# Kernel optimization log

Hardware: AMD Instinct MI355X
Metric: run time of the kernel (lower is better)

Reference implementation:

```python
import jax, jax.numpy as jnp
import numpy as np

N_NODES = 50000
N_EDGES = 800000
D_FEAT = 128
D_EMB = 128


def _spmm(row, col, val, x, n):
    # y[i] = sum_{e: row[e]==i} val[e] * x[col[e]]  -- COO spmm via gather + segment_sum
    return jax.ops.segment_sum(val[:, None] * x[col], row, num_segments=n)


def setup_inputs() -> dict:
    key = jax.random.key(0)
    k1, k2, k3, k4, k5 = jax.random.split(key, 5)
    feature = jax.random.normal(k1, (N_NODES, D_FEAT), dtype=jnp.float32)
    adj_row = jax.random.randint(k2, (N_EDGES,), 0, N_NODES, dtype=jnp.int32)
    adj_col = jax.random.randint(k3, (N_EDGES,), 0, N_NODES, dtype=jnp.int32)
    adj_val = jax.random.uniform(k4, (N_EDGES,), dtype=jnp.float32)
    stdv = 1.0 / np.sqrt(D_EMB)
    weight = jax.random.uniform(k5, (D_FEAT, D_EMB), minval=-stdv, maxval=stdv, dtype=jnp.float32)
    return {"feature": feature, "adj_row": adj_row, "adj_col": adj_col,
            "adj_val": adj_val, "weight": weight}


def reference(feature, adj_row, adj_col, adj_val, weight):
    n = feature.shape[0]
    h = _spmm(adj_row, adj_col, adj_val, feature, n)   # adj @ feature
    h = _spmm(adj_row, adj_col, adj_val, h, n)         # adj @ (adj @ feature)
    out = 0.5 * h - 0.5 * feature                      # elementwise combine
    return out @ weight                                # dense projection [N, D_EMB]
```

## Files before the change

### kernel.cpp

```cpp
#include <hip/hip_runtime.h>
#include <hip/hip_fp16.h>

#define D 128
#define SCAT_EPT 16
#define CAP 48

typedef _Float16 f16;
typedef f16 f16x8 __attribute__((ext_vector_type(8)));
typedef float f32x4 __attribute__((ext_vector_type(4)));


__global__ __launch_bounds__(256) void conv_init_kernel(
    const float* __restrict__ x, __half* __restrict__ xh,
    const float* __restrict__ W, __half* __restrict__ Wt,
    int* __restrict__ cnt, long n8, int N) {
  long i = (long)blockIdx.x * blockDim.x + threadIdx.x;
  if (i < n8) {
    const float4* src = reinterpret_cast<const float4*>(x) + i * 2;
    float4 a = src[0], b = src[1];
    __half2 h0 = __floats2half2_rn(a.x, a.y);
    __half2 h1 = __floats2half2_rn(a.z, a.w);
    __half2 h2 = __floats2half2_rn(b.x, b.y);
    __half2 h3 = __floats2half2_rn(b.z, b.w);
    uint4 st;
    st.x = *reinterpret_cast<uint*>(&h0);
    st.y = *reinterpret_cast<uint*>(&h1);
    st.z = *reinterpret_cast<uint*>(&h2);
    st.w = *reinterpret_cast<uint*>(&h3);
    *(reinterpret_cast<uint4*>(xh) + i) = st;
  }
  if (i < D * D) {
    int k = (int)(i >> 7), j = (int)(i & 127);
    Wt[((long)j << 7) + k] = __float2half_rn(W[i]);
  }
  if (i < N) cnt[i] = 0;
}


__global__ __launch_bounds__(256) void build_part_kernel(
    const int* __restrict__ row, const int* __restrict__ col,
    const float* __restrict__ val, int* __restrict__ cnt,
    int2* __restrict__ csrB, int E, int N) {
  const int g = blockIdx.x & 7;
  const int chunk = blockIdx.x >> 3;
  const int gsize = (N + 7) >> 3;
  const int rlo = g * gsize;
  const int rhi = rlo + gsize;
  int i = chunk * (256 * SCAT_EPT) + threadIdx.x;
#pragma unroll
  for (int t = 0; t < SCAT_EPT; ++t, i += 256) {
    if (i < E) {
      int r = row[i];
      if (r >= rlo && r < rhi) {
        int p = atomicAdd(&cnt[r], 1);
        if (p < CAP) csrB[(long)r * CAP + p] = make_int2(col[i], __float_as_int(val[i]));
      }
    }
  }
}


__device__ __forceinline__ float2 row_accum_wave(const int2* __restrict__ cv,
                                                 long s, long e,
                                                 const __half* __restrict__ xh,
                                                 int lane) {
  float2 acc = {0.f, 0.f};
  const int loff = lane << 1;
  long k = s;
  const long e8 = s + ((e - s) & ~7L);
  for (; k < e8; k += 8) {
    int2 c0 = cv[k + 0], c1 = cv[k + 1], c2 = cv[k + 2], c3 = cv[k + 3];
    int2 c4 = cv[k + 4], c5 = cv[k + 5], c6 = cv[k + 6], c7 = cv[k + 7];
    uint u0 = *reinterpret_cast<const uint*>(xh + ((long)c0.x << 7) + loff);
    uint u1 = *reinterpret_cast<const uint*>(xh + ((long)c1.x << 7) + loff);
    uint u2 = *reinterpret_cast<const uint*>(xh + ((long)c2.x << 7) + loff);
    uint u3 = *reinterpret_cast<const uint*>(xh + ((long)c3.x << 7) + loff);
    uint u4 = *reinterpret_cast<const uint*>(xh + ((long)c4.x << 7) + loff);
    uint u5 = *reinterpret_cast<const uint*>(xh + ((long)c5.x << 7) + loff);
    uint u6 = *reinterpret_cast<const uint*>(xh + ((long)c6.x << 7) + loff);
    uint u7 = *reinterpret_cast<const uint*>(xh + ((long)c7.x << 7) + loff);
#define ACC1(uu, cc)                                            \
    {                                                           \
      __half2 h = *reinterpret_cast<__half2*>(&(uu));           \
      float2 f = __half22float2(h);                             \
      float v = __int_as_float((cc).y);                         \
      acc.x = fmaf(v, f.x, acc.x);                              \
      acc.y = fmaf(v, f.y, acc.y);                              \
    }
    ACC1(u0, c0) ACC1(u1, c1) ACC1(u2, c2) ACC1(u3, c3)
    ACC1(u4, c4) ACC1(u5, c5) ACC1(u6, c6) ACC1(u7, c7)
  }
  for (; k < e; ++k) {
    int2 c = cv[k];
    uint u = *reinterpret_cast<const uint*>(xh + ((long)c.x << 7) + loff);
    ACC1(u, c)
  }
#undef ACC1
  return acc;
}


__global__ __launch_bounds__(256) void spmm1_kernel(
    const int* __restrict__ cnt, const int2* __restrict__ csrB,
    const __half* __restrict__ xh, __half* __restrict__ y, int N) {
  int r = blockIdx.x * 4 + (threadIdx.x >> 6);
  int lane = threadIdx.x & 63;
  if (r >= N) return;
  int deg = __builtin_amdgcn_readfirstlane(min(cnt[r], CAP));
  long s = (long)r * CAP;
  float2 acc = row_accum_wave(csrB, s, s + deg, xh, lane);
  __half2 p = __floats2half2_rn(acc.x, acc.y);
  *reinterpret_cast<__half2*>(y + ((long)r << 7) + (lane << 1)) = p;
}


__global__ __launch_bounds__(256) void spmm2z_kernel(
    const int* __restrict__ cnt, const int2* __restrict__ csrB,
    const __half* __restrict__ h1, const float* __restrict__ feat,
    __half* __restrict__ zh, int N) {
  int r = blockIdx.x * 4 + (threadIdx.x >> 6);
  int lane = threadIdx.x & 63;
  if (r >= N) return;
  int deg = __builtin_amdgcn_readfirstlane(min(cnt[r], CAP));
  long s = (long)r * CAP;
  float2 acc = row_accum_wave(csrB, s, s + deg, h1, lane);
  float2 fv = *reinterpret_cast<const float2*>(feat + ((long)r << 7) + (lane << 1));
  __half2 p = __floats2half2_rn(0.5f * (acc.x - fv.x), 0.5f * (acc.y - fv.y));
  *reinterpret_cast<__half2*>(zh + ((long)r << 7) + (lane << 1)) = p;
}


__global__ __launch_bounds__(256) void gemmz_mfma_kernel(
    const __half* __restrict__ zh, const __half* __restrict__ Wt,
    float* __restrict__ out, int N) {
  const int w = threadIdx.x >> 6;
  const int l = threadIdx.x & 63;
  const int r0 = blockIdx.x * 64 + w * 16;
  const int lr = l & 15;
  const int lk = (l >> 4) * 8;

  f16x8 a[4];
  const f16* zp = reinterpret_cast<const f16*>(zh) + ((long)(r0 + lr) << 7) + lk;
#pragma unroll
  for (int ks = 0; ks < 4; ++ks)
    a[ks] = *reinterpret_cast<const f16x8*>(zp + ks * 32);

  const int orow = r0 + (l >> 4) * 4;
#pragma unroll
  for (int jt = 0; jt < 8; ++jt) {
    const f16* wp = reinterpret_cast<const f16*>(Wt) + ((long)(jt * 16 + lr) << 7) + lk;
    f16x8 b0 = *reinterpret_cast<const f16x8*>(wp + 0);
    f16x8 b1 = *reinterpret_cast<const f16x8*>(wp + 32);
    f16x8 b2 = *reinterpret_cast<const f16x8*>(wp + 64);
    f16x8 b3 = *reinterpret_cast<const f16x8*>(wp + 96);
    f32x4 acc = {0.f, 0.f, 0.f, 0.f};
    acc = __builtin_amdgcn_mfma_f32_16x16x32_f16(a[0], b0, acc, 0, 0, 0);
    acc = __builtin_amdgcn_mfma_f32_16x16x32_f16(a[1], b1, acc, 0, 0, 0);
    acc = __builtin_amdgcn_mfma_f32_16x16x32_f16(a[2], b2, acc, 0, 0, 0);
    acc = __builtin_amdgcn_mfma_f32_16x16x32_f16(a[3], b3, acc, 0, 0, 0);
#pragma unroll
    for (int i = 0; i < 4; ++i) {
      int r = orow + i;
      if (r < N) out[((long)r << 7) + jt * 16 + lr] = acc[i];
    }
  }
}


__global__ __launch_bounds__(256) void spmm_atomic_kernel(
    const int* __restrict__ row, const int* __restrict__ col,
    const float* __restrict__ val, const float* __restrict__ x,
    float* __restrict__ y, int E) {
  long idx = (long)blockIdx.x * blockDim.x + threadIdx.x;
  int e = (int)(idx >> 5);
  if (e >= E) return;
  int q = (int)(idx & 31);
  int r = row[e];
  int c = col[e];
  float v = val[e];
  const float4 xv = *reinterpret_cast<const float4*>(x + (long)c * D + q * 4);
  float* yp = y + (long)r * D + q * 4;
  atomicAdd(yp + 0, v * xv.x);
  atomicAdd(yp + 1, v * xv.y);
  atomicAdd(yp + 2, v * xv.z);
  atomicAdd(yp + 3, v * xv.w);
}

__global__ __launch_bounds__(256) void combine_gemm_kernel(
    const float* __restrict__ h2, const float* __restrict__ feat,
    const float* __restrict__ W, float* __restrict__ out, int N) {
  __shared__ float Xs[32][D];
  const int t = threadIdx.x;
  const int rb = blockIdx.x * 32;
#pragma unroll
  for (int i = 0; i < 4; ++i) {
    int o = i * 1024 + t * 4;
    int r = o >> 7;
    int cc = o & 127;
    float4 xv = {0.f, 0.f, 0.f, 0.f};
    if (rb + r < N) {
      float4 hv = *reinterpret_cast<const float4*>(h2 + (long)(rb + r) * D + cc);
      float4 fv = *reinterpret_cast<const float4*>(feat + (long)(rb + r) * D + cc);
      xv.x = 0.5f * (hv.x - fv.x);
      xv.y = 0.5f * (hv.y - fv.y);
      xv.z = 0.5f * (hv.z - fv.z);
      xv.w = 0.5f * (hv.w - fv.w);
    }
    *reinterpret_cast<float4*>(&Xs[r][cc]) = xv;
  }
  __syncthreads();
  const int j0 = (t & 31) * 4;
  const int i0 = (t >> 5) * 4;
  float4 acc[4];
#pragma unroll
  for (int ii = 0; ii < 4; ++ii) acc[ii] = {0.f, 0.f, 0.f, 0.f};
#pragma unroll 8
  for (int kb = 0; kb < 32; ++kb) {
    float4 xr[4], wr[4];
#pragma unroll
    for (int ii = 0; ii < 4; ++ii)
      xr[ii] = *reinterpret_cast<const float4*>(&Xs[i0 + ii][kb * 4]);
#pragma unroll
    for (int kk = 0; kk < 4; ++kk)
      wr[kk] = *reinterpret_cast<const float4*>(W + (kb * 4 + kk) * D + j0);
#pragma unroll
    for (int ii = 0; ii < 4; ++ii) {
      const float* xp = &xr[ii].x;
#pragma unroll
      for (int kk = 0; kk < 4; ++kk) {
        float xk = xp[kk];
        acc[ii].x = fmaf(xk, wr[kk].x, acc[ii].x);
        acc[ii].y = fmaf(xk, wr[kk].y, acc[ii].y);
        acc[ii].z = fmaf(xk, wr[kk].z, acc[ii].z);
        acc[ii].w = fmaf(xk, wr[kk].w, acc[ii].w);
      }
    }
  }
#pragma unroll
  for (int ii = 0; ii < 4; ++ii) {
    int r = rb + i0 + ii;
    if (r < N)
      *reinterpret_cast<float4*>(out + (long)r * D + j0) = acc[ii];
  }
}


static inline size_t align256(size_t x) { return (x + 255) & ~(size_t)255; }

extern "C" void kernel_launch(void* const* d_in, const int* in_sizes, int n_in,
                              void* d_out, int out_size, void* d_ws, size_t ws_size,
                              hipStream_t stream) {
  const float* feature = (const float*)d_in[0];
  const int* adj_row   = (const int*)d_in[1];
  const int* adj_col   = (const int*)d_in[2];
  const float* adj_val = (const float*)d_in[3];
  const float* weight  = (const float*)d_in[4];
  float* out = (float*)d_out;

  const int N = in_sizes[0] / D;
  const int E = in_sizes[1];
  const size_t hbytes  = (size_t)N * D * sizeof(float);
  const size_t hbytes2 = (size_t)N * D * sizeof(__half);

  char* p = (char*)d_ws;
  int* cnt       = (int*)p;    p += align256((size_t)N * 4);
  __half* wt     = (__half*)p; p += align256((size_t)D * D * 2);
  int2* csrB     = (int2*)p;   p += align256((size_t)N * CAP * 8);
  __half* feath  = (__half*)p; p += align256(hbytes2);
  const size_t need = (size_t)(p - (char*)d_ws);

  if (ws_size >= need) {
    __half* h1h = (__half*)d_out;
    const long n8 = (long)N * D / 8;
    conv_init_kernel<<<(int)((n8 + 255) / 256), 256, 0, stream>>>(
        feature, feath, weight, wt, cnt, n8, N);
    const int chunks = (E + 256 * SCAT_EPT - 1) / (256 * SCAT_EPT);
    build_part_kernel<<<chunks * 8, 256, 0, stream>>>(adj_row, adj_col, adj_val,
                                                      cnt, csrB, E, N);
    spmm1_kernel<<<(N + 3) / 4, 256, 0, stream>>>(cnt, csrB, feath, h1h, N);
    spmm2z_kernel<<<(N + 3) / 4, 256, 0, stream>>>(cnt, csrB, h1h, feature,
                                                   feath, N);
    gemmz_mfma_kernel<<<(N + 63) / 64, 256, 0, stream>>>(feath, wt, out, N);
  } else {
    float* fh1 = out;
    float* fh2 = (float*)d_ws;
    const long items = (long)E * 32;
    const int spmm_blocks = (int)((items + 255) / 256);
    hipMemsetAsync(fh1, 0, hbytes, stream);
    spmm_atomic_kernel<<<spmm_blocks, 256, 0, stream>>>(adj_row, adj_col, adj_val,
                                                        feature, fh1, E);
    hipMemsetAsync(fh2, 0, hbytes, stream);
    spmm_atomic_kernel<<<spmm_blocks, 256, 0, stream>>>(adj_row, adj_col, adj_val,
                                                        fh1, fh2, E);
    combine_gemm_kernel<<<(N + 31) / 32, 256, 0, stream>>>(fh2, feature, weight,
                                                           out, N);
  }
}
```

Baseline: 151.2 us.

## Merge feature conversion with CSR build and deepen gather unroll to 16

The fp16 conversion of features and weights is fused into the CSR-bucket build kernel as extra leading blocks, so both run in one launch. The counter zeroing moves to a hipMemsetAsync, which is needed because the build blocks now run alongside conversion. The row-gather loop is unrolled to 16 edges with an 8-edge step before the scalar tail, giving more loads in flight per wave. The trade-off is higher register pressure in the gather loop and an extra memset call replacing the zeroing that was folded in before.

Result: slower. 158.3 us (+4.7%).

```diff
diff --git a/kernel.cpp b/kernel.cpp
--- a/kernel.cpp
+++ b/kernel.cpp
@@ -10,39 +10,37 @@
 typedef float f32x4 __attribute__((ext_vector_type(4)));
 
 
-__global__ __launch_bounds__(256) void conv_init_kernel(
+__global__ __launch_bounds__(256) void conv_build_kernel(
     const float* __restrict__ x, __half* __restrict__ xh,
     const float* __restrict__ W, __half* __restrict__ Wt,
-    int* __restrict__ cnt, long n8, int N) {
-  long i = (long)blockIdx.x * blockDim.x + threadIdx.x;
-  if (i < n8) {
-    const float4* src = reinterpret_cast<const float4*>(x) + i * 2;
-    float4 a = src[0], b = src[1];
-    __half2 h0 = __floats2half2_rn(a.x, a.y);
-    __half2 h1 = __floats2half2_rn(a.z, a.w);
-    __half2 h2 = __floats2half2_rn(b.x, b.y);
-    __half2 h3 = __floats2half2_rn(b.z, b.w);
-    uint4 st;
-    st.x = *reinterpret_cast<uint*>(&h0);
-    st.y = *reinterpret_cast<uint*>(&h1);
-    st.z = *reinterpret_cast<uint*>(&h2);
-    st.w = *reinterpret_cast<uint*>(&h3);
-    *(reinterpret_cast<uint4*>(xh) + i) = st;
-  }
-  if (i < D * D) {
-    int k = (int)(i >> 7), j = (int)(i & 127);
-    Wt[((long)j << 7) + k] = __float2half_rn(W[i]);
-  }
-  if (i < N) cnt[i] = 0;
-}
-
-
-__global__ __launch_bounds__(256) void build_part_kernel(
     const int* __restrict__ row, const int* __restrict__ col,
     const float* __restrict__ val, int* __restrict__ cnt,
-    int2* __restrict__ csrB, int E, int N) {
-  const int g = blockIdx.x & 7;
-  const int chunk = blockIdx.x >> 3;
+    int2* __restrict__ csrB, long n8, int E, int N, int convB) {
+  if ((int)blockIdx.x < convB) {
+    long i = (long)blockIdx.x * blockDim.x + threadIdx.x;
+    if (i < n8) {
+      const float4* src = reinterpret_cast<const float4*>(x) + i * 2;
+      float4 a = src[0], b = src[1];
+      __half2 h0 = __floats2half2_rn(a.x, a.y);
+      __half2 h1 = __floats2half2_rn(a.z, a.w);
+      __half2 h2 = __floats2half2_rn(b.x, b.y);
+      __half2 h3 = __floats2half2_rn(b.z, b.w);
+      uint4 st;
+      st.x = *reinterpret_cast<uint*>(&h0);
+      st.y = *reinterpret_cast<uint*>(&h1);
+      st.z = *reinterpret_cast<uint*>(&h2);
+      st.w = *reinterpret_cast<uint*>(&h3);
+      *(reinterpret_cast<uint4*>(xh) + i) = st;
+    }
+    if (i < D * D) {
+      int k = (int)(i >> 7), j = (int)(i & 127);
+      Wt[((long)j << 7) + k] = __float2half_rn(W[i]);
+    }
+    return;
+  }
+  const int bid = (int)blockIdx.x - convB;
+  const int g = bid & 7;
+  const int chunk = bid >> 3;
   const int gsize = (N + 7) >> 3;
   const int rlo = g * gsize;
   const int rhi = rlo + gsize;
@@ -67,35 +65,50 @@
   float2 acc = {0.f, 0.f};
   const int loff = lane << 1;
   long k = s;
-  const long e8 = s + ((e - s) & ~7L);
-  for (; k < e8; k += 8) {
-    int2 c0 = cv[k + 0], c1 = cv[k + 1], c2 = cv[k + 2], c3 = cv[k + 3];
-    int2 c4 = cv[k + 4], c5 = cv[k + 5], c6 = cv[k + 6], c7 = cv[k + 7];
-    uint u0 = *reinterpret_cast<const uint*>(xh + ((long)c0.x << 7) + loff);
-    uint u1 = *reinterpret_cast<const uint*>(xh + ((long)c1.x << 7) + loff);
-    uint u2 = *reinterpret_cast<const uint*>(xh + ((long)c2.x << 7) + loff);
-    uint u3 = *reinterpret_cast<const uint*>(xh + ((long)c3.x << 7) + loff);
-    uint u4 = *reinterpret_cast<const uint*>(xh + ((long)c4.x << 7) + loff);
-    uint u5 = *reinterpret_cast<const uint*>(xh + ((long)c5.x << 7) + loff);
-    uint u6 = *reinterpret_cast<const uint*>(xh + ((long)c6.x << 7) + loff);
-    uint u7 = *reinterpret_cast<const uint*>(xh + ((long)c7.x << 7) + loff);
-#define ACC1(uu, cc)                                            \
-    {                                                           \
-      __half2 h = *reinterpret_cast<__half2*>(&(uu));           \
-      float2 f = __half22float2(h);                             \
-      float v = __int_as_float((cc).y);                         \
-      acc.x = fmaf(v, f.x, acc.x);                              \
-      acc.y = fmaf(v, f.y, acc.y);                              \
-    }
-    ACC1(u0, c0) ACC1(u1, c1) ACC1(u2, c2) ACC1(u3, c3)
-    ACC1(u4, c4) ACC1(u5, c5) ACC1(u6, c6) ACC1(u7, c7)
+  for (; k + 16 <= e; k += 16) {
+    int2 c[16];
+    uint u[16];
+#pragma unroll
+    for (int j = 0; j < 16; ++j) c[j] = cv[k + j];
+#pragma unroll
+    for (int j = 0; j < 16; ++j)
+      u[j] = *reinterpret_cast<const uint*>(xh + ((long)c[j].x << 7) + loff);
+#pragma unroll
+    for (int j = 0; j < 16; ++j) {
+      __half2 h = *reinterpret_cast<__half2*>(&u[j]);
+      float2 f = __half22float2(h);
+      float v = __int_as_float(c[j].y);
+      acc.x = fmaf(v, f.x, acc.x);
+      acc.y = fmaf(v, f.y, acc.y);
+    }
+  }
+  if (k + 8 <= e) {
+    int2 c[8];
+    uint u[8];
+#pragma unroll
+    for (int j = 0; j < 8; ++j) c[j] = cv[k + j];
+#pragma unroll
+    for (int j = 0; j < 8; ++j)
+      u[j] = *reinterpret_cast<const uint*>(xh + ((long)c[j].x << 7) + loff);
+#pragma unroll
+    for (int j = 0; j < 8; ++j) {
+      __half2 h = *reinterpret_cast<__half2*>(&u[j]);
+      float2 f = __half22float2(h);
+      float v = __int_as_float(c[j].y);
+      acc.x = fmaf(v, f.x, acc.x);
+      acc.y = fmaf(v, f.y, acc.y);
+    }
+    k += 8;
   }
   for (; k < e; ++k) {
     int2 c = cv[k];
-    uint u = *reinterpret_cast<const uint*>(xh + ((long)c.x << 7) + loff);
-    ACC1(u, c)
-  }
-#undef ACC1
+    uint uu = *reinterpret_cast<const uint*>(xh + ((long)c.x << 7) + loff);
+    __half2 h = *reinterpret_cast<__half2*>(&uu);
+    float2 f = __half22float2(h);
+    float v = __int_as_float(c.y);
+    acc.x = fmaf(v, f.x, acc.x);
+    acc.y = fmaf(v, f.y, acc.y);
+  }
   return acc;
 }
 
@@ -272,11 +285,12 @@
   if (ws_size >= need) {
     __half* h1h = (__half*)d_out;
     const long n8 = (long)N * D / 8;
-    conv_init_kernel<<<(int)((n8 + 255) / 256), 256, 0, stream>>>(
-        feature, feath, weight, wt, cnt, n8, N);
+    const int convB = (int)((n8 + 255) / 256);
     const int chunks = (E + 256 * SCAT_EPT - 1) / (256 * SCAT_EPT);
-    build_part_kernel<<<chunks * 8, 256, 0, stream>>>(adj_row, adj_col, adj_val,
-                                                      cnt, csrB, E, N);
+    hipMemsetAsync(cnt, 0, (size_t)N * 4, stream);
+    conv_build_kernel<<<convB + chunks * 8, 256, 0, stream>>>(
+        feature, feath, weight, wt, adj_row, adj_col, adj_val,
+        cnt, csrB, n8, E, N, convB);
     spmm1_kernel<<<(N + 3) / 4, 256, 0, stream>>>(cnt, csrB, feath, h1h, N);
     spmm2z_kernel<<<(N + 3) / 4, 256, 0, stream>>>(cnt, csrB, h1h, feature,
                                                    feath, N);
```

## Build padded CSR via two-pass bucketed scatter with shared-memory atomics

Applied to the files above, without the earlier changes.

Replaces the global-atomic per-row scatter, which read the edge list eight times, with a two-phase build. Pass one counts edges into 512-row buckets using shared-memory atomics, reserves ranges with one global atomic per bucket, and writes packed staging entries into the output buffer. Pass two works per bucket and scatters those entries into per-row slots with shared-memory counters. The f16 conversion is merged into the first kernel's launch. This trades an extra staging pass and fixed capacity limits (CB per bucket, N < 65536 for the 16-bit column packing) for far fewer global atomics and edge reads.

Result: faster. 147.3 us (-2.6%).

```diff
diff --git a/kernel.cpp b/kernel.cpp
--- a/kernel.cpp
+++ b/kernel.cpp
@@ -2,60 +2,99 @@
 #include <hip/hip_fp16.h>
 
 #define D 128
-#define SCAT_EPT 16
 #define CAP 48
+#define NBMAX 128
+#define BSHIFT 9
+#define CB 9216
+#define EPB 4096
 
 typedef _Float16 f16;
 typedef f16 f16x8 __attribute__((ext_vector_type(8)));
 typedef float f32x4 __attribute__((ext_vector_type(4)));
 
 
-__global__ __launch_bounds__(256) void conv_init_kernel(
+__global__ __launch_bounds__(256) void conv_p1_kernel(
     const float* __restrict__ x, __half* __restrict__ xh,
     const float* __restrict__ W, __half* __restrict__ Wt,
-    int* __restrict__ cnt, long n8, int N) {
-  long i = (long)blockIdx.x * blockDim.x + threadIdx.x;
-  if (i < n8) {
-    const float4* src = reinterpret_cast<const float4*>(x) + i * 2;
-    float4 a = src[0], b = src[1];
-    __half2 h0 = __floats2half2_rn(a.x, a.y);
-    __half2 h1 = __floats2half2_rn(a.z, a.w);
-    __half2 h2 = __floats2half2_rn(b.x, b.y);
-    __half2 h3 = __floats2half2_rn(b.z, b.w);
-    uint4 st;
-    st.x = *reinterpret_cast<uint*>(&h0);
-    st.y = *reinterpret_cast<uint*>(&h1);
-    st.z = *reinterpret_cast<uint*>(&h2);
-    st.w = *reinterpret_cast<uint*>(&h3);
-    *(reinterpret_cast<uint4*>(xh) + i) = st;
-  }
-  if (i < D * D) {
-    int k = (int)(i >> 7), j = (int)(i & 127);
-    Wt[((long)j << 7) + k] = __float2half_rn(W[i]);
-  }
-  if (i < N) cnt[i] = 0;
-}
-
-
-__global__ __launch_bounds__(256) void build_part_kernel(
     const int* __restrict__ row, const int* __restrict__ col,
-    const float* __restrict__ val, int* __restrict__ cnt,
-    int2* __restrict__ csrB, int E, int N) {
-  const int g = blockIdx.x & 7;
-  const int chunk = blockIdx.x >> 3;
-  const int gsize = (N + 7) >> 3;
-  const int rlo = g * gsize;
-  const int rhi = rlo + gsize;
-  int i = chunk * (256 * SCAT_EPT) + threadIdx.x;
-#pragma unroll
-  for (int t = 0; t < SCAT_EPT; ++t, i += 256) {
+    const float* __restrict__ val, int* __restrict__ bcur,
+    int2* __restrict__ staging, long n8, int E, int nchunks) {
+  if ((int)blockIdx.x >= nchunks) {
+    long i = (long)((int)blockIdx.x - nchunks) * 256 + threadIdx.x;
+    if (i < n8) {
+      const float4* src = reinterpret_cast<const float4*>(x) + i * 2;
+      float4 a = src[0], b = src[1];
+      __half2 h0 = __floats2half2_rn(a.x, a.y);
+      __half2 h1 = __floats2half2_rn(a.z, a.w);
+      __half2 h2 = __floats2half2_rn(b.x, b.y);
+      __half2 h3 = __floats2half2_rn(b.z, b.w);
+      uint4 st;
+      st.x = *reinterpret_cast<uint*>(&h0);
+      st.y = *reinterpret_cast<uint*>(&h1);
+      st.z = *reinterpret_cast<uint*>(&h2);
+      st.w = *reinterpret_cast<uint*>(&h3);
+      *(reinterpret_cast<uint4*>(xh) + i) = st;
+    }
+    if (i < D * D) {
+      int k = (int)(i >> 7), j = (int)(i & 127);
+      Wt[((long)j << 7) + k] = __float2half_rn(W[i]);
+    }
+    return;
+  }
+  __shared__ int bcnt[NBMAX];
+  __shared__ int bbase[NBMAX];
+  const int t = threadIdx.x;
+  for (int b = t; b < NBMAX; b += 256) bcnt[b] = 0;
+  __syncthreads();
+  const int e0 = (int)blockIdx.x * EPB;
+#pragma unroll
+  for (int j = 0; j < EPB / 256; ++j) {
+    int i = e0 + j * 256 + t;
+    if (i < E) atomicAdd(&bcnt[row[i] >> BSHIFT], 1);
+  }
+  __syncthreads();
+  for (int b = t; b < NBMAX; b += 256) {
+    int c = bcnt[b];
+    bbase[b] = (c > 0) ? atomicAdd(&bcur[b], c) : 0;
+    bcnt[b] = 0;
+  }
+  __syncthreads();
+#pragma unroll
+  for (int j = 0; j < EPB / 256; ++j) {
+    int i = e0 + j * 256 + t;
     if (i < E) {
       int r = row[i];
-      if (r >= rlo && r < rhi) {
-        int p = atomicAdd(&cnt[r], 1);
-        if (p < CAP) csrB[(long)r * CAP + p] = make_int2(col[i], __float_as_int(val[i]));
-      }
-    }
+      int b = r >> BSHIFT;
+      int p = atomicAdd(&bcnt[b], 1) + bbase[b];
+      if (p < CB)
+        staging[(long)b * CB + p] =
+            make_int2(((r & 511) << 16) | col[i], __float_as_int(val[i]));
+    }
+  }
+}
+
+
+__global__ __launch_bounds__(256) void p2_kernel(
+    const int* __restrict__ bcur, const int2* __restrict__ staging,
+    int* __restrict__ cnt, int2* __restrict__ csrB, int N) {
+  const int b = blockIdx.x;
+  const int rlo = b << BSHIFT;
+  __shared__ int rc[512];
+  const int t = threadIdx.x;
+  for (int j = t; j < 512; j += 256) rc[j] = 0;
+  __syncthreads();
+  const int cntE = min(bcur[b], CB);
+  for (int i = t; i < cntE; i += 256) {
+    int2 e = staging[(long)b * CB + i];
+    int rloc = e.x >> 16;
+    int c = e.x & 0xFFFF;
+    int p = atomicAdd(&rc[rloc], 1);
+    if (p < CAP) csrB[(long)(rlo + rloc) * CAP + p] = make_int2(c, e.y);
+  }
+  __syncthreads();
+  for (int j = t; j < 512; j += 256) {
+    int r = rlo + j;
+    if (r < N) cnt[r] = rc[j];
   }
 }
 
@@ -261,22 +300,29 @@
   const int E = in_sizes[1];
   const size_t hbytes  = (size_t)N * D * sizeof(float);
   const size_t hbytes2 = (size_t)N * D * sizeof(__half);
+  const int nb = (N + 511) >> BSHIFT;
 
   char* p = (char*)d_ws;
+  int* bcur      = (int*)p;    p += align256((size_t)NBMAX * 4);
   int* cnt       = (int*)p;    p += align256((size_t)N * 4);
   __half* wt     = (__half*)p; p += align256((size_t)D * D * 2);
   int2* csrB     = (int2*)p;   p += align256((size_t)N * CAP * 8);
   __half* feath  = (__half*)p; p += align256(hbytes2);
   const size_t need = (size_t)(p - (char*)d_ws);
-
-  if (ws_size >= need) {
+  const size_t stage_need = hbytes2 + (size_t)nb * CB * 8;
+
+  if (ws_size >= need && nb <= NBMAX && N < 65536 &&
+      stage_need <= (size_t)out_size * 4) {
     __half* h1h = (__half*)d_out;
+    int2* staging = (int2*)((char*)d_out + hbytes2);
     const long n8 = (long)N * D / 8;
-    conv_init_kernel<<<(int)((n8 + 255) / 256), 256, 0, stream>>>(
-        feature, feath, weight, wt, cnt, n8, N);
-    const int chunks = (E + 256 * SCAT_EPT - 1) / (256 * SCAT_EPT);
-    build_part_kernel<<<chunks * 8, 256, 0, stream>>>(adj_row, adj_col, adj_val,
-                                                      cnt, csrB, E, N);
+    const int convB = (int)((n8 + 255) / 256);
+    const int nchunks = (E + EPB - 1) / EPB;
+    hipMemsetAsync(bcur, 0, (size_t)NBMAX * 4, stream);
+    conv_p1_kernel<<<nchunks + convB, 256, 0, stream>>>(
+        feature, feath, weight, wt, adj_row, adj_col, adj_val,
+        bcur, staging, n8, E, nchunks);
+    p2_kernel<<<nb, 256, 0, stream>>>(bcur, staging, cnt, csrB, N);
     spmm1_kernel<<<(N + 3) / 4, 256, 0, stream>>>(cnt, csrB, feath, h1h, N);
     spmm2z_kernel<<<(N + 3) / 4, 256, 0, stream>>>(cnt, csrB, h1h, feature,
                                                    feath, N);
```
